# Kernel optimization log

Measured on AMD Instinct MI355X. Metric: run time of the kernel, lower is better.

## Reference

```python
import jax, jax.numpy as jnp
import numpy as np

B = 96   # batch (must equal C for the residual broadcast to be legal)
C = 96   # num_channels == seq_len (x is (B, C, 1, C))
S = 96   # sequence length = C
NH = 8   # num_heads
DK = 96  # d_k (defaults to num_channels)
G = 8    # groupnorm groups
EPS = 1e-5


def setup_inputs() -> dict:
    key = jax.random.key(0)
    ks = jax.random.split(key, 9)
    D = NH * DK
    scale = 0.05
    return {
        "x": jax.random.normal(ks[0], (B, C, 1, C), jnp.float32),
        "Wq": jax.random.normal(ks[1], (C, D), jnp.float32) * scale,
        "bq": jax.random.normal(ks[2], (D,), jnp.float32) * scale,
        "Wk": jax.random.normal(ks[3], (C, D), jnp.float32) * scale,
        "bk": jax.random.normal(ks[4], (D,), jnp.float32) * scale,
        "Wv": jax.random.normal(ks[5], (C, D), jnp.float32) * scale,
        "bv": jax.random.normal(ks[6], (D,), jnp.float32) * scale,
        "Wo": jax.random.normal(ks[7], (D, C), jnp.float32) * scale,
        "bo": jax.random.normal(ks[8], (C,), jnp.float32) * scale,
        "gamma": jnp.ones((C,), jnp.float32),
        "beta": jnp.zeros((C,), jnp.float32),
    }


def group_norm(x, gamma, beta):
    # x: (B, C, H, W); normalize over (C//G, H, W) within each of G groups
    b, c, h, w = x.shape
    xg = x.reshape(b, G, -1)
    mu = jnp.mean(xg, axis=-1, keepdims=True)
    var = jnp.var(xg, axis=-1, keepdims=True)
    xn = ((xg - mu) * jax.lax.rsqrt(var + EPS)).reshape(b, c, h, w)
    return xn * gamma[None, :, None, None] + beta[None, :, None, None]


def reference(x, Wq, bq, Wk, bk, Wv, bv, Wo, bo, gamma, beta):
    xn = group_norm(x, gamma, beta)           # (B, C, 1, C)
    residual = xn
    t = xn.reshape(B, S, C)                   # H == 1, squeeze
    # self-attention: q = k = v = normalized x
    q = (t @ Wq + bq).reshape(B, S, NH, DK).transpose(0, 2, 1, 3)  # (B, H, S, Dk)
    k = (t @ Wk + bk).reshape(B, S, NH, DK).transpose(0, 2, 1, 3)
    v = (t @ Wv + bv).reshape(B, S, NH, DK).transpose(0, 2, 1, 3)
    scores = jnp.einsum('bhqd,bhkd->bhqk', q, k) / jnp.sqrt(jnp.float32(DK))
    causal = jnp.tril(jnp.ones((S, S), bool))  # mask=True -> causal tril mask
    scores = jnp.where(causal[None, None], scores, -jnp.inf)
    attn = jax.nn.softmax(scores, axis=-1)
    out = jnp.einsum('bhqk,bhkd->bhqd', attn, v)       # (B, H, S, Dk)
    out = out.transpose(0, 2, 1, 3).reshape(B, S, NH * DK)
    out = out @ Wo + bo                                # (B, S, C); dropout(p=0) = id
    # faithful to the source: (B,S,C) + (B,C,1,C) broadcasts to (B,C,S,C)
    return out + residual
```

## Files before the change

### kernel.cpp

```cpp
#include <hip/hip_runtime.h>
#include <hip/hip_bf16.h>

#define BATCH 96
#define CH    96
#define SEQ   96
#define NHEAD 8
#define DK    96
#define DMODEL 768
#define GRP   8
#define EPSV  1e-5f

typedef __bf16 bf16x8 __attribute__((ext_vector_type(8)));
typedef float  f32x4  __attribute__((ext_vector_type(4)));
typedef unsigned short u16;

__device__ __forceinline__ u16 f2bf(float f) {
    union { float f; unsigned int u; } c; c.f = f;
    unsigned int u = c.u + 0x7fffu + ((c.u >> 16) & 1u);
    return (u16)(u >> 16);
}

__global__ __launch_bounds__(128) void gn_kernel(
        const float* __restrict__ x, const float* __restrict__ gamma,
        const float* __restrict__ beta, float* __restrict__ xn,
        u16* __restrict__ xn_bf) {
    int bg = blockIdx.x;
    int b = bg >> 3, g = bg & 7;
    const float* xp = x + b * 9216 + g * 1152;
    float vals[9];
    float s = 0.f, ss = 0.f;
    #pragma unroll
    for (int r = 0; r < 9; ++r) {
        float v = xp[threadIdx.x + 128 * r];
        vals[r] = v; s += v; ss += v * v;
    }
    #pragma unroll
    for (int off = 32; off > 0; off >>= 1) {
        s  += __shfl_down(s, off);
        ss += __shfl_down(ss, off);
    }
    __shared__ float red[4];
    if ((threadIdx.x & 63) == 0) {
        red[(threadIdx.x >> 6) * 2]     = s;
        red[(threadIdx.x >> 6) * 2 + 1] = ss;
    }
    __syncthreads();
    s = red[0] + red[2]; ss = red[1] + red[3];
    float mu   = s * (1.0f / 1152.0f);
    float var  = ss * (1.0f / 1152.0f) - mu * mu;
    float rsig = rsqrtf(var + EPSV);
    #pragma unroll
    for (int r = 0; r < 9; ++r) {
        int e = threadIdx.x + 128 * r;
        int c = g * 12 + e / 96;
        float v = (vals[r] - mu) * rsig * gamma[c] + beta[c];
        int idx = b * 9216 + g * 1152 + e;
        xn[idx]    = v;
        xn_bf[idx] = f2bf(v);
    }
}

__global__ __launch_bounds__(256) void wconv_kernel(
        const float* __restrict__ Wq, const float* __restrict__ Wk,
        const float* __restrict__ Wv, const float* __restrict__ Wo,
        u16* __restrict__ WqT, u16* __restrict__ WkT,
        u16* __restrict__ WvT, u16* __restrict__ WoT) {
    int seg = blockIdx.y;
    const float* src = seg == 0 ? Wq : seg == 1 ? Wk : seg == 2 ? Wv : Wo;
    u16* dst = seg == 0 ? WqT : seg == 1 ? WkT : seg == 2 ? WvT : WoT;
    int idx = blockIdx.x * 256 + threadIdx.x;
    if (idx < 73728) {
        if (seg < 3) {
            int n = idx / 96, k2 = idx - n * 96;
            dst[idx] = f2bf(src[k2 * 768 + n]);
        } else {
            int n = idx / 768, k2 = idx - n * 768;
            dst[idx] = f2bf(src[k2 * 96 + n]);
        }
    }
}

__global__ __launch_bounds__(256) void qkv_kernel(
        const u16* __restrict__ xn_bf,
        const u16* __restrict__ WqT, const u16* __restrict__ WkT,
        const u16* __restrict__ WvT,
        const float* __restrict__ bq, const float* __restrict__ bk,
        const float* __restrict__ bv,
        u16* __restrict__ q, u16* __restrict__ k, u16* __restrict__ v) {
    int z = blockIdx.z;
    const u16* WT = z == 0 ? WqT : z == 1 ? WkT : WvT;
    const float* bias = z == 0 ? bq : z == 1 ? bk : bv;
    u16* out = z == 0 ? q : z == 1 ? k : v;

    int wave = threadIdx.x >> 6, lane = threadIdx.x & 63;
    int ln = lane & 15, quad = lane >> 4;
    int m0 = blockIdx.x * 128 + (wave >> 1) * 64;
    int n0 = blockIdx.y * 128 + (wave & 1) * 64;

    f32x4 acc[4][4] = {};
    #pragma unroll
    for (int kt = 0; kt < 3; ++kt) {
        bf16x8 a[4], bb[4];
        #pragma unroll
        for (int mt = 0; mt < 4; ++mt)
            a[mt] = *(const bf16x8*)(xn_bf + (m0 + mt * 16 + ln) * 96 + kt * 32 + quad * 8);
        #pragma unroll
        for (int nt = 0; nt < 4; ++nt)
            bb[nt] = *(const bf16x8*)(WT + (n0 + nt * 16 + ln) * 96 + kt * 32 + quad * 8);
        #pragma unroll
        for (int mt = 0; mt < 4; ++mt)
            #pragma unroll
            for (int nt = 0; nt < 4; ++nt)
                acc[mt][nt] = __builtin_amdgcn_mfma_f32_16x16x32_bf16(
                    a[mt], bb[nt], acc[mt][nt], 0, 0, 0);
    }
    #pragma unroll
    for (int mt = 0; mt < 4; ++mt) {
        int row = m0 + mt * 16 + quad * 4;
        #pragma unroll
        for (int nt = 0; nt < 4; ++nt) {
            int col = n0 + nt * 16 + ln;
            float bcol = bias[col];
            #pragma unroll
            for (int r = 0; r < 4; ++r)
                out[(size_t)(row + r) * DMODEL + col] = f2bf(acc[mt][nt][r] + bcol);
        }
    }
}

__global__ __launch_bounds__(384) void attn_kernel(
        const u16* __restrict__ q, const u16* __restrict__ k,
        const u16* __restrict__ v, u16* __restrict__ attn_out) {
    int b = blockIdx.x >> 3, h = blockIdx.x & 7;
    __shared__ __align__(16) u16 vt[96][104];
    __shared__ __align__(16) u16 pP[96][104];
    const size_t base = (size_t)b * 96 * DMODEL + h * 96;

    for (int idx = threadIdx.x; idx < 9216; idx += 384) {
        int s = idx / 96, d = idx - s * 96;
        vt[d][s] = v[base + (size_t)s * DMODEL + d];
    }

    int wave = threadIdx.x >> 6, lane = threadIdx.x & 63;
    int ln = lane & 15, quad = lane >> 4;

    f32x4 accs[6] = {};
    #pragma unroll
    for (int kt = 0; kt < 3; ++kt) {
        bf16x8 a = *(const bf16x8*)(q + base + (size_t)(wave * 16 + ln) * DMODEL + kt * 32 + quad * 8);
        #pragma unroll
        for (int nt = 0; nt < 6; ++nt) {
            bf16x8 bb = *(const bf16x8*)(k + base + (size_t)(nt * 16 + ln) * DMODEL + kt * 32 + quad * 8);
            accs[nt] = __builtin_amdgcn_mfma_f32_16x16x32_bf16(a, bb, accs[nt], 0, 0, 0);
        }
    }

    const float scale = 0.10206207261596577f;
    #pragma unroll
    for (int r = 0; r < 4; ++r) {
        int row = wave * 16 + quad * 4 + r;
        float vals[6], m = -1e30f;
        #pragma unroll
        for (int nt = 0; nt < 6; ++nt) {
            int col = nt * 16 + ln;
            float sv = accs[nt][r] * scale;
            vals[nt] = (col <= row) ? sv : -1e30f;
            m = fmaxf(m, vals[nt]);
        }
        #pragma unroll
        for (int off = 1; off < 16; off <<= 1) m = fmaxf(m, __shfl_xor(m, off));
        float p[6], sum = 0.f;
        #pragma unroll
        for (int nt = 0; nt < 6; ++nt) {
            p[nt] = (vals[nt] > -1e29f) ? __expf(vals[nt] - m) : 0.f;
            sum += p[nt];
        }
        #pragma unroll
        for (int off = 1; off < 16; off <<= 1) sum += __shfl_xor(sum, off);
        float rinv = 1.0f / sum;
        #pragma unroll
        for (int nt = 0; nt < 6; ++nt)
            pP[row][nt * 16 + ln] = f2bf(p[nt] * rinv);
    }
    __syncthreads();

    f32x4 acco[6] = {};
    #pragma unroll
    for (int kt = 0; kt < 3; ++kt) {
        bf16x8 a = *(const bf16x8*)(&pP[wave * 16 + ln][kt * 32 + quad * 8]);
        #pragma unroll
        for (int nt = 0; nt < 6; ++nt) {
            bf16x8 bb = *(const bf16x8*)(&vt[nt * 16 + ln][kt * 32 + quad * 8]);
            acco[nt] = __builtin_amdgcn_mfma_f32_16x16x32_bf16(a, bb, acco[nt], 0, 0, 0);
        }
    }
    #pragma unroll
    for (int nt = 0; nt < 6; ++nt) {
        int d = nt * 16 + ln;
        #pragma unroll
        for (int r = 0; r < 4; ++r) {
            int row = wave * 16 + quad * 4 + r;
            attn_out[base + (size_t)row * DMODEL + d] = f2bf(acco[nt][r]);
        }
    }
}

__global__ __launch_bounds__(256) void oproj_kernel(
        const u16* __restrict__ attn, const u16* __restrict__ WoT,
        const float* __restrict__ bo, float* __restrict__ proj) {
    int wave = threadIdx.x >> 6, lane = threadIdx.x & 63;
    int ln = lane & 15, quad = lane >> 4;
    int m0 = (blockIdx.x * 4 + wave) * 16;
    f32x4 acc[6] = {};
    #pragma unroll 4
    for (int kt = 0; kt < 24; ++kt) {
        bf16x8 a = *(const bf16x8*)(attn + (size_t)(m0 + ln) * DMODEL + kt * 32 + quad * 8);
        #pragma unroll
        for (int nt = 0; nt < 6; ++nt) {
            bf16x8 bb = *(const bf16x8*)(WoT + (nt * 16 + ln) * DMODEL + kt * 32 + quad * 8);
            acc[nt] = __builtin_amdgcn_mfma_f32_16x16x32_bf16(a, bb, acc[nt], 0, 0, 0);
        }
    }
    int row = m0 + quad * 4;
    #pragma unroll
    for (int nt = 0; nt < 6; ++nt) {
        int col = nt * 16 + ln;
        float bb = bo[col];
        #pragma unroll
        for (int r = 0; r < 4; ++r)
            proj[(row + r) * 96 + col] = acc[nt][r] + bb;
    }
}

__global__ __launch_bounds__(256) void bcast_kernel(
        const float* __restrict__ proj, const float* __restrict__ xn,
        float* __restrict__ out) {
    int i = blockIdx.x / 96, j = blockIdx.x - i * 96;
    __shared__ float4 xrow[24];
    if (threadIdx.x < 24)
        xrow[threadIdx.x] = ((const float4*)(xn + (i * 96 + j) * 96))[threadIdx.x];
    __syncthreads();
    const float4* p4 = (const float4*)proj + j * 2304;
    float4* o4 = (float4*)out + (size_t)(i * 96 + j) * 2304;
    #pragma unroll
    for (int it = 0; it < 9; ++it) {
        int idx = threadIdx.x + it * 256;
        int kk = idx / 24;
        int l4 = idx - kk * 24;
        float4 pv = p4[idx];
        float4 xv = xrow[l4];
        float4 rr;
        rr.x = pv.x + xv.x; rr.y = pv.y + xv.y;
        rr.z = pv.z + xv.z; rr.w = pv.w + xv.w;
        o4[idx] = rr;
    }
}

extern "C" void kernel_launch(void* const* d_in, const int* in_sizes, int n_in,
                              void* d_out, int out_size, void* d_ws, size_t ws_size,
                              hipStream_t stream) {
    const float* x     = (const float*)d_in[0];
    const float* Wq    = (const float*)d_in[1];
    const float* bq    = (const float*)d_in[2];
    const float* Wk    = (const float*)d_in[3];
    const float* bk    = (const float*)d_in[4];
    const float* Wv    = (const float*)d_in[5];
    const float* bv    = (const float*)d_in[6];
    const float* Wo    = (const float*)d_in[7];
    const float* bo    = (const float*)d_in[8];
    const float* gamma = (const float*)d_in[9];
    const float* beta  = (const float*)d_in[10];
    float* out = (float*)d_out;

    char* ws = (char*)d_ws;
    float* xn_f = (float*)(ws + 0);
    u16*  xn_b  = (u16*)(ws + 3538944);
    u16*  WqT   = (u16*)(ws + 5308416);
    u16*  WkT   = (u16*)(ws + 5455872);
    u16*  WvT   = (u16*)(ws + 5603328);
    u16*  WoT   = (u16*)(ws + 5750784);
    u16*  qb    = (u16*)(ws + 5898240);
    u16*  kb    = (u16*)(ws + 20054016);
    u16*  vb    = (u16*)(ws + 34209792);
    u16*  ab    = (u16*)(ws + 48365568);
    float* proj = (float*)(ws + 62521344);

    gn_kernel<<<dim3(BATCH * GRP), dim3(128), 0, stream>>>(x, gamma, beta, xn_f, xn_b);
    wconv_kernel<<<dim3(288, 4), dim3(256), 0, stream>>>(Wq, Wk, Wv, Wo, WqT, WkT, WvT, WoT);
    qkv_kernel<<<dim3(72, 6, 3), dim3(256), 0, stream>>>(xn_b, WqT, WkT, WvT,
                                                         bq, bk, bv, qb, kb, vb);
    attn_kernel<<<dim3(BATCH * NHEAD), dim3(384), 0, stream>>>(qb, kb, vb, ab);
    oproj_kernel<<<dim3(144), dim3(256), 0, stream>>>(ab, WoT, bo, proj);
    bcast_kernel<<<dim3(96 * 96), dim3(256), 0, stream>>>(proj, xn_f, out);
}
```

Baseline: 433.6 us.

## Fuse QKV projection into attention kernel and split-K the output projection

Result: no change. 428.8 us (-1.1%).

```diff
diff --git a/kernel.cpp b/kernel.cpp
--- a/kernel.cpp
+++ b/kernel.cpp
@@ -13,6 +13,8 @@
 typedef __bf16 bf16x8 __attribute__((ext_vector_type(8)));
 typedef float  f32x4  __attribute__((ext_vector_type(4)));
 typedef unsigned short u16;
+
+#define MFMA16(a, b, c) __builtin_amdgcn_mfma_f32_16x16x32_bf16((a), (b), (c), 0, 0, 0)
 
 __device__ __forceinline__ u16 f2bf(float f) {
     union { float f; unsigned int u; } c; c.f = f;
@@ -80,85 +82,76 @@
     }
 }
 
-__global__ __launch_bounds__(256) void qkv_kernel(
+__global__ __launch_bounds__(384) void fattn_kernel(
         const u16* __restrict__ xn_bf,
         const u16* __restrict__ WqT, const u16* __restrict__ WkT,
         const u16* __restrict__ WvT,
         const float* __restrict__ bq, const float* __restrict__ bk,
         const float* __restrict__ bv,
-        u16* __restrict__ q, u16* __restrict__ k, u16* __restrict__ v) {
-    int z = blockIdx.z;
-    const u16* WT = z == 0 ? WqT : z == 1 ? WkT : WvT;
-    const float* bias = z == 0 ? bq : z == 1 ? bk : bv;
-    u16* out = z == 0 ? q : z == 1 ? k : v;
+        u16* __restrict__ attn_out) {
+    int b = blockIdx.x >> 3, h = blockIdx.x & 7;
+    __shared__ __align__(16) u16 qb[96][104];
+    __shared__ __align__(16) u16 kb[96][104];
+    __shared__ __align__(16) u16 vt[96][104];
 
     int wave = threadIdx.x >> 6, lane = threadIdx.x & 63;
     int ln = lane & 15, quad = lane >> 4;
-    int m0 = blockIdx.x * 128 + (wave >> 1) * 64;
-    int n0 = blockIdx.y * 128 + (wave & 1) * 64;
-
-    f32x4 acc[4][4] = {};
-    #pragma unroll
-    for (int kt = 0; kt < 3; ++kt) {
-        bf16x8 a[4], bb[4];
-        #pragma unroll
-        for (int mt = 0; mt < 4; ++mt)
-            a[mt] = *(const bf16x8*)(xn_bf + (m0 + mt * 16 + ln) * 96 + kt * 32 + quad * 8);
-        #pragma unroll
-        for (int nt = 0; nt < 4; ++nt)
-            bb[nt] = *(const bf16x8*)(WT + (n0 + nt * 16 + ln) * 96 + kt * 32 + quad * 8);
-        #pragma unroll
-        for (int mt = 0; mt < 4; ++mt)
-            #pragma unroll
-            for (int nt = 0; nt < 4; ++nt)
-                acc[mt][nt] = __builtin_amdgcn_mfma_f32_16x16x32_bf16(
-                    a[mt], bb[nt], acc[mt][nt], 0, 0, 0);
-    }
-    #pragma unroll
-    for (int mt = 0; mt < 4; ++mt) {
-        int row = m0 + mt * 16 + quad * 4;
-        #pragma unroll
-        for (int nt = 0; nt < 4; ++nt) {
-            int col = n0 + nt * 16 + ln;
-            float bcol = bias[col];
-            #pragma unroll
-            for (int r = 0; r < 4; ++r)
-                out[(size_t)(row + r) * DMODEL + col] = f2bf(acc[mt][nt][r] + bcol);
-        }
-    }
-}
-
-__global__ __launch_bounds__(384) void attn_kernel(
-        const u16* __restrict__ q, const u16* __restrict__ k,
-        const u16* __restrict__ v, u16* __restrict__ attn_out) {
-    int b = blockIdx.x >> 3, h = blockIdx.x & 7;
-    __shared__ __align__(16) u16 vt[96][104];
-    __shared__ __align__(16) u16 pP[96][104];
-    const size_t base = (size_t)b * 96 * DMODEL + h * 96;
-
-    for (int idx = threadIdx.x; idx < 9216; idx += 384) {
-        int s = idx / 96, d = idx - s * 96;
-        vt[d][s] = v[base + (size_t)s * DMODEL + d];
-    }
-
-    int wave = threadIdx.x >> 6, lane = threadIdx.x & 63;
-    int ln = lane & 15, quad = lane >> 4;
+    int m0 = wave * 16;
+    const u16* xb = xn_bf + b * 9216;
+    const int hq = h * 96;
+
+    bf16x8 a[3], av[3];
+    #pragma unroll
+    for (int kt = 0; kt < 3; ++kt) {
+        a[kt]  = *(const bf16x8*)(xb + (m0 + ln) * 96 + kt * 32 + quad * 8);
+        av[kt] = *(const bf16x8*)(WvT + (hq + m0 + ln) * 96 + kt * 32 + quad * 8);
+    }
+    f32x4 aq[6] = {}, ak[6] = {}, avv[6] = {};
+    #pragma unroll
+    for (int kt = 0; kt < 3; ++kt) {
+        #pragma unroll
+        for (int nt = 0; nt < 6; ++nt) {
+            bf16x8 bqf = *(const bf16x8*)(WqT + (hq + nt * 16 + ln) * 96 + kt * 32 + quad * 8);
+            aq[nt] = MFMA16(a[kt], bqf, aq[nt]);
+            bf16x8 bkf = *(const bf16x8*)(WkT + (hq + nt * 16 + ln) * 96 + kt * 32 + quad * 8);
+            ak[nt] = MFMA16(a[kt], bkf, ak[nt]);
+            bf16x8 bvf = *(const bf16x8*)(xb + (nt * 16 + ln) * 96 + kt * 32 + quad * 8);
+            avv[nt] = MFMA16(av[kt], bvf, avv[nt]);
+        }
+    }
+    float bvr[4];
+    #pragma unroll
+    for (int r = 0; r < 4; ++r) bvr[r] = bv[hq + m0 + quad * 4 + r];
+    #pragma unroll
+    for (int nt = 0; nt < 6; ++nt) {
+        int col = nt * 16 + ln;
+        float bqc = bq[hq + col], bkc = bk[hq + col];
+        #pragma unroll
+        for (int r = 0; r < 4; ++r) {
+            int row = m0 + quad * 4 + r;
+            qb[row][col] = f2bf(aq[nt][r] + bqc);
+            kb[row][col] = f2bf(ak[nt][r] + bkc);
+            vt[row][col] = f2bf(avv[nt][r] + bvr[r]);
+        }
+    }
+    __syncthreads();
 
     f32x4 accs[6] = {};
     #pragma unroll
     for (int kt = 0; kt < 3; ++kt) {
-        bf16x8 a = *(const bf16x8*)(q + base + (size_t)(wave * 16 + ln) * DMODEL + kt * 32 + quad * 8);
-        #pragma unroll
-        for (int nt = 0; nt < 6; ++nt) {
-            bf16x8 bb = *(const bf16x8*)(k + base + (size_t)(nt * 16 + ln) * DMODEL + kt * 32 + quad * 8);
-            accs[nt] = __builtin_amdgcn_mfma_f32_16x16x32_bf16(a, bb, accs[nt], 0, 0, 0);
+        bf16x8 aa = *(const bf16x8*)(&qb[m0 + ln][kt * 32 + quad * 8]);
+        #pragma unroll
+        for (int nt = 0; nt < 6; ++nt) {
+            bf16x8 bb = *(const bf16x8*)(&kb[nt * 16 + ln][kt * 32 + quad * 8]);
+            accs[nt] = MFMA16(aa, bb, accs[nt]);
         }
     }
 
     const float scale = 0.10206207261596577f;
+    float pout[4][6];
     #pragma unroll
     for (int r = 0; r < 4; ++r) {
-        int row = wave * 16 + quad * 4 + r;
+        int row = m0 + quad * 4 + r;
         float vals[6], m = -1e30f;
         #pragma unroll
         for (int nt = 0; nt < 6; ++nt) {
@@ -169,38 +162,44 @@
         }
         #pragma unroll
         for (int off = 1; off < 16; off <<= 1) m = fmaxf(m, __shfl_xor(m, off));
-        float p[6], sum = 0.f;
-        #pragma unroll
-        for (int nt = 0; nt < 6; ++nt) {
-            p[nt] = (vals[nt] > -1e29f) ? __expf(vals[nt] - m) : 0.f;
-            sum += p[nt];
+        float sum = 0.f;
+        #pragma unroll
+        for (int nt = 0; nt < 6; ++nt) {
+            float p = (vals[nt] > -1e29f) ? __expf(vals[nt] - m) : 0.f;
+            pout[r][nt] = p; sum += p;
         }
         #pragma unroll
         for (int off = 1; off < 16; off <<= 1) sum += __shfl_xor(sum, off);
         float rinv = 1.0f / sum;
         #pragma unroll
+        for (int nt = 0; nt < 6; ++nt) pout[r][nt] *= rinv;
+    }
+    __syncthreads();
+    #pragma unroll
+    for (int r = 0; r < 4; ++r)
+        #pragma unroll
         for (int nt = 0; nt < 6; ++nt)
-            pP[row][nt * 16 + ln] = f2bf(p[nt] * rinv);
-    }
+            kb[m0 + quad * 4 + r][nt * 16 + ln] = f2bf(pout[r][nt]);
     __syncthreads();
 
     f32x4 acco[6] = {};
     #pragma unroll
     for (int kt = 0; kt < 3; ++kt) {
-        bf16x8 a = *(const bf16x8*)(&pP[wave * 16 + ln][kt * 32 + quad * 8]);
+        bf16x8 aa = *(const bf16x8*)(&kb[m0 + ln][kt * 32 + quad * 8]);
         #pragma unroll
         for (int nt = 0; nt < 6; ++nt) {
             bf16x8 bb = *(const bf16x8*)(&vt[nt * 16 + ln][kt * 32 + quad * 8]);
-            acco[nt] = __builtin_amdgcn_mfma_f32_16x16x32_bf16(a, bb, acco[nt], 0, 0, 0);
-        }
-    }
+            acco[nt] = MFMA16(aa, bb, acco[nt]);
+        }
+    }
+    const size_t obase = (size_t)b * 96 * DMODEL + hq;
     #pragma unroll
     for (int nt = 0; nt < 6; ++nt) {
         int d = nt * 16 + ln;
         #pragma unroll
         for (int r = 0; r < 4; ++r) {
-            int row = wave * 16 + quad * 4 + r;
-            attn_out[base + (size_t)row * DMODEL + d] = f2bf(acco[nt][r]);
+            int row = m0 + quad * 4 + r;
+            attn_out[obase + (size_t)row * DMODEL + d] = f2bf(acco[nt][r]);
         }
     }
 }
@@ -210,25 +209,32 @@
         const float* __restrict__ bo, float* __restrict__ proj) {
     int wave = threadIdx.x >> 6, lane = threadIdx.x & 63;
     int ln = lane & 15, quad = lane >> 4;
-    int m0 = (blockIdx.x * 4 + wave) * 16;
+    int m0 = blockIdx.x * 16;
+    int k0 = wave * 192;
     f32x4 acc[6] = {};
-    #pragma unroll 4
-    for (int kt = 0; kt < 24; ++kt) {
-        bf16x8 a = *(const bf16x8*)(attn + (size_t)(m0 + ln) * DMODEL + kt * 32 + quad * 8);
-        #pragma unroll
-        for (int nt = 0; nt < 6; ++nt) {
-            bf16x8 bb = *(const bf16x8*)(WoT + (nt * 16 + ln) * DMODEL + kt * 32 + quad * 8);
-            acc[nt] = __builtin_amdgcn_mfma_f32_16x16x32_bf16(a, bb, acc[nt], 0, 0, 0);
-        }
-    }
-    int row = m0 + quad * 4;
-    #pragma unroll
-    for (int nt = 0; nt < 6; ++nt) {
-        int col = nt * 16 + ln;
-        float bb = bo[col];
+    #pragma unroll
+    for (int kt = 0; kt < 6; ++kt) {
+        bf16x8 a = *(const bf16x8*)(attn + (size_t)(m0 + ln) * DMODEL + k0 + kt * 32 + quad * 8);
+        #pragma unroll
+        for (int nt = 0; nt < 6; ++nt) {
+            bf16x8 bb = *(const bf16x8*)(WoT + (nt * 16 + ln) * DMODEL + k0 + kt * 32 + quad * 8);
+            acc[nt] = MFMA16(a, bb, acc[nt]);
+        }
+    }
+    __shared__ float red[4][16][96];
+    #pragma unroll
+    for (int nt = 0; nt < 6; ++nt)
         #pragma unroll
         for (int r = 0; r < 4; ++r)
-            proj[(row + r) * 96 + col] = acc[nt][r] + bb;
+            red[wave][quad * 4 + r][nt * 16 + ln] = acc[nt][r];
+    __syncthreads();
+    #pragma unroll
+    for (int e = 0; e < 6; ++e) {
+        int idx = threadIdx.x + e * 256;
+        int row = idx / 96, col = idx - row * 96;
+        float s = red[0][row][col] + red[1][row][col] +
+                  red[2][row][col] + red[3][row][col] + bo[col];
+        proj[(m0 + row) * 96 + col] = s;
     }
 }
 
@@ -279,17 +285,13 @@
     u16*  WkT   = (u16*)(ws + 5455872);
     u16*  WvT   = (u16*)(ws + 5603328);
     u16*  WoT   = (u16*)(ws + 5750784);
-    u16*  qb    = (u16*)(ws + 5898240);
-    u16*  kb    = (u16*)(ws + 20054016);
-    u16*  vb    = (u16*)(ws + 34209792);
-    u16*  ab    = (u16*)(ws + 48365568);
-    float* proj = (float*)(ws + 62521344);
+    u16*  ab    = (u16*)(ws + 5898240);
+    float* proj = (float*)(ws + 20054016);
 
     gn_kernel<<<dim3(BATCH * GRP), dim3(128), 0, stream>>>(x, gamma, beta, xn_f, xn_b);
     wconv_kernel<<<dim3(288, 4), dim3(256), 0, stream>>>(Wq, Wk, Wv, Wo, WqT, WkT, WvT, WoT);
-    qkv_kernel<<<dim3(72, 6, 3), dim3(256), 0, stream>>>(xn_b, WqT, WkT, WvT,
-                                                         bq, bk, bv, qb, kb, vb);
-    attn_kernel<<<dim3(BATCH * NHEAD), dim3(384), 0, stream>>>(qb, kb, vb, ab);
-    oproj_kernel<<<dim3(144), dim3(256), 0, stream>>>(ab, WoT, bo, proj);
+    fattn_kernel<<<dim3(BATCH * NHEAD), dim3(384), 0, stream>>>(
+        xn_b, WqT, WkT, WvT, bq, bk, bv, ab);
+    oproj_kernel<<<dim3(576), dim3(256), 0, stream>>>(ab, WoT, bo, proj);
     bcast_kernel<<<dim3(96 * 96), dim3(256), 0, stream>>>(proj, xn_f, out);
 }
```
